# Kernel optimization log

Measured on AMD Instinct MI355X. Metric: run time of the kernel, lower is better.

The kernel has to match this reference:

```python
import jax, jax.numpy as jnp
import numpy as np

NUM_HEADS = 16
NEG = -1e9


def setup_inputs() -> dict:
    key = jax.random.key(0)
    ks = jax.random.split(key, 9)
    B, S, D = 1, 4096, 1024
    s = 1.0 / np.sqrt(D)
    return {
        "x": jax.random.normal(ks[0], (B, S, D), dtype=jnp.float32),
        "wq": jax.random.normal(ks[1], (D, D), dtype=jnp.float32) * s,
        "bq": jax.random.normal(ks[2], (D,), dtype=jnp.float32) * s,
        "wk": jax.random.normal(ks[3], (D, D), dtype=jnp.float32) * s,
        "bk": jax.random.normal(ks[4], (D,), dtype=jnp.float32) * s,
        "wv": jax.random.normal(ks[5], (D, D), dtype=jnp.float32) * s,
        "bv": jax.random.normal(ks[6], (D,), dtype=jnp.float32) * s,
        "wo": jax.random.normal(ks[7], (D, D), dtype=jnp.float32) * s,
        "bo": jax.random.normal(ks[8], (D,), dtype=jnp.float32) * s,
    }


def reference(x, wq, bq, wk, bk, wv, bv, wo, bo):
    B, S, D = x.shape
    H = NUM_HEADS
    hs = D // H
    # torch Linear: y = x @ W^T + b
    q = x @ wq.T + bq
    k = x @ wk.T + bk
    v = x @ wv.T + bv
    # [B, S, D] -> [B, H, S, hs]
    q = q.reshape(B, S, H, hs).transpose(0, 2, 1, 3)
    k = k.reshape(B, S, H, hs).transpose(0, 2, 1, 3)
    v = v.reshape(B, S, H, hs).transpose(0, 2, 1, 3)
    scores = jnp.einsum("bhqd,bhkd->bhqk", q, k) / jnp.sqrt(jnp.asarray(hs, x.dtype))
    causal = jnp.tril(jnp.ones((S, S), dtype=bool))  # True = keep
    scores = jnp.where(causal, scores, jnp.asarray(NEG, x.dtype))
    weights = jax.nn.softmax(scores, axis=-1)
    out = jnp.einsum("bhqk,bhkd->bhqd", weights, v)
    out = out.transpose(0, 2, 1, 3).reshape(B, S, D)
    return out @ wo.T + bo
```

## Files before the change

kernel.cpp:

```cpp
#include <hip/hip_runtime.h>

#define SEQ 4096
#define DM  1024
#define NH  16
#define HS  64
#define LDQK 2048

typedef __attribute__((ext_vector_type(8))) _Float16 f16x8;
typedef __attribute__((ext_vector_type(4))) _Float16 f16x4;
typedef __attribute__((ext_vector_type(4))) float    f32x4;

#define MFMA16(a, b, c) __builtin_amdgcn_mfma_f32_16x16x32_f16((a), (b), (c), 0, 0, 0)

#define DPP_ROR_F(x, N) __int_as_float(__builtin_amdgcn_update_dpp( \
    0, __float_as_int(x), 0x120 + (N), 0xF, 0xF, false))

__device__ __forceinline__ float red16_add(float x) {
    x += DPP_ROR_F(x, 1);
    x += DPP_ROR_F(x, 2);
    x += DPP_ROR_F(x, 4);
    x += DPP_ROR_F(x, 8);
    return x;
}

__global__ __launch_bounds__(256) void cast_all(
    const float* __restrict__ x,
    const float* __restrict__ wq, const float* __restrict__ wk,
    const float* __restrict__ wv, const float* __restrict__ wo,
    _Float16* __restrict__ xb, _Float16* __restrict__ wqkb,
    _Float16* __restrict__ wvb, _Float16* __restrict__ wob)
{
    const float* s; _Float16* d; int i;
    if (blockIdx.y == 0) {
        s = x; d = xb;
        i = blockIdx.x * 1024 + threadIdx.x * 4;
    } else {
        int wsel = blockIdx.x >> 10;
        int bx   = blockIdx.x & 1023;
        switch (wsel) {
            case 0:  s = wq; d = wqkb;               break;
            case 1:  s = wk; d = wqkb + (1u << 20);  break;
            case 2:  s = wv; d = wvb;                break;
            default: s = wo; d = wob;                break;
        }
        i = bx * 1024 + threadIdx.x * 4;
    }
    float4 v = *reinterpret_cast<const float4*>(s + i);
    f16x4 o = {(_Float16)v.x, (_Float16)v.y, (_Float16)v.z, (_Float16)v.w};
    *reinterpret_cast<f16x4*>(d + i) = o;
}

#define GPAD 72

template <int BIAS_ROW, typename OUT_T>
__global__ __launch_bounds__(256, 2) void gemm_bt_f16(
    const _Float16* __restrict__ A,
    const _Float16* __restrict__ W,
    const float*    __restrict__ bias_lo,
    const float*    __restrict__ bias_hi,
    OUT_T* __restrict__ C,
    int M, int N, int K,
    float scale_lo, float scale_hi, int nsplit)
{
    __shared__ _Float16 As[64][GPAD];
    __shared__ _Float16 Bs[128][GPAD];

    const int t    = threadIdx.x;
    const int w    = t >> 6;
    const int lane = t & 63;
    const int q    = lane >> 4;
    const int l    = lane & 15;
    const int m0   = blockIdx.y * 64;
    const int n0   = blockIdx.x * 128;
    const int wm   = (w & 1) * 32;
    const int wn   = (w >> 1) * 64;

    const float* bias  = (n0 < nsplit) ? bias_lo : bias_hi;
    const int    nbase = (n0 < nsplit) ? 0 : nsplit;
    const float  scale = (n0 < nsplit) ? scale_lo : scale_hi;

    const int ar = t >> 2, ac = (t & 3) * 16;
    const int br = t >> 1, bc = (t & 1) * 32;
    const _Float16* gA = A + (size_t)(m0 + ar) * K + ac;
    const _Float16* gW = W + (size_t)(n0 + br) * K + bc;

    uint4 ra0 = *reinterpret_cast<const uint4*>(gA);
    uint4 ra1 = *reinterpret_cast<const uint4*>(gA + 8);
    uint4 rb0 = *reinterpret_cast<const uint4*>(gW);
    uint4 rb1 = *reinterpret_cast<const uint4*>(gW + 8);
    uint4 rb2 = *reinterpret_cast<const uint4*>(gW + 16);
    uint4 rb3 = *reinterpret_cast<const uint4*>(gW + 24);

    f32x4 acc[2][4];
    #pragma unroll
    for (int i = 0; i < 2; ++i)
        #pragma unroll
        for (int j = 0; j < 4; ++j) acc[i][j] = (f32x4){0.f, 0.f, 0.f, 0.f};

    for (int k0 = 0; k0 < K; k0 += 64) {
        __syncthreads();
        *reinterpret_cast<uint4*>(&As[ar][ac])      = ra0;
        *reinterpret_cast<uint4*>(&As[ar][ac + 8])  = ra1;
        *reinterpret_cast<uint4*>(&Bs[br][bc])      = rb0;
        *reinterpret_cast<uint4*>(&Bs[br][bc + 8])  = rb1;
        *reinterpret_cast<uint4*>(&Bs[br][bc + 16]) = rb2;
        *reinterpret_cast<uint4*>(&Bs[br][bc + 24]) = rb3;
        if (k0 + 64 < K) {
            ra0 = *reinterpret_cast<const uint4*>(gA + k0 + 64);
            ra1 = *reinterpret_cast<const uint4*>(gA + k0 + 72);
            rb0 = *reinterpret_cast<const uint4*>(gW + k0 + 64);
            rb1 = *reinterpret_cast<const uint4*>(gW + k0 + 72);
            rb2 = *reinterpret_cast<const uint4*>(gW + k0 + 80);
            rb3 = *reinterpret_cast<const uint4*>(gW + k0 + 88);
        }
        __syncthreads();

        #pragma unroll
        for (int ks = 0; ks < 64; ks += 32) {
            f16x8 af[2], bf[4];
            #pragma unroll
            for (int i = 0; i < 2; ++i)
                af[i] = *reinterpret_cast<const f16x8*>(&As[wm + i * 16 + l][ks + q * 8]);
            #pragma unroll
            for (int j = 0; j < 4; ++j)
                bf[j] = *reinterpret_cast<const f16x8*>(&Bs[wn + j * 16 + l][ks + q * 8]);
            #pragma unroll
            for (int i = 0; i < 2; ++i)
                #pragma unroll
                for (int j = 0; j < 4; ++j)
                    acc[i][j] = MFMA16(af[i], bf[j], acc[i][j]);
        }
    }

    #pragma unroll
    for (int i = 0; i < 2; ++i) {
        #pragma unroll
        for (int j = 0; j < 4; ++j) {
            int gnb = n0 + wn + j * 16 + l;
            float bc2 = BIAS_ROW ? 0.f : bias[gnb - nbase];
            #pragma unroll
            for (int r = 0; r < 4; ++r) {
                int gm = m0 + wm + i * 16 + q * 4 + r;
                float bb = BIAS_ROW ? bias[gm] : bc2;
                C[(size_t)gm * N + gnb] = (OUT_T)((acc[i][j][r] + bb) * scale);
            }
        }
    }
}

#define APAD 72

__global__ __launch_bounds__(256, 2) void attn_mfma(
    const _Float16* __restrict__ Qg,
    const _Float16* __restrict__ Kg,
    const _Float16* __restrict__ Vt,
    _Float16* __restrict__ O)
{
    __shared__ _Float16 QP[128][APAD];
    __shared__ _Float16 Ks[4][16][APAD];
    __shared__ _Float16 Vs[64][APAD];

    const int t    = threadIdx.x;
    const int h    = blockIdx.x;
    const int by   = blockIdx.y;
    const int qb   = (by < 16) ? by : 47 - by;
    const int w    = t >> 6;
    const int lane = t & 63;
    const int q    = lane >> 4;
    const int l    = lane & 15;
    const int sr   = t >> 3;
    const int sc   = (t & 7) * 8;
    const int kj   = sr & 3;
    const int kn   = sr >> 2;

    #pragma unroll
    for (int rr = 0; rr < 4; ++rr)
        *reinterpret_cast<uint4*>(&QP[sr + rr * 32][sc]) =
            *reinterpret_cast<const uint4*>(
                Qg + (size_t)(qb * 128 + sr + rr * 32) * LDQK + h * 64 + sc);

    uint4 kr0 = *reinterpret_cast<const uint4*>(Kg + (size_t)(sr) * LDQK + h * 64 + sc);
    uint4 kr1 = *reinterpret_cast<const uint4*>(Kg + (size_t)(sr + 32) * LDQK + h * 64 + sc);
    uint4 vr0 = *reinterpret_cast<const uint4*>(Vt + (size_t)(h * 64 + sr) * SEQ + sc);
    uint4 vr1 = *reinterpret_cast<const uint4*>(Vt + (size_t)(h * 64 + sr + 32) * SEQ + sc);

    float l_acc[2][4];
    f32x4 oacc[2][4];
    #pragma unroll
    for (int i = 0; i < 2; ++i)
        #pragma unroll
        for (int nt = 0; nt < 4; ++nt) {
            oacc[i][nt] = (f32x4){0.f, 0.f, 0.f, 0.f};
            l_acc[i][nt] = 0.f;
        }

    __syncthreads();
    f16x8 aq[2][2];
    #pragma unroll
    for (int i = 0; i < 2; ++i) {
        aq[i][0] = *reinterpret_cast<const f16x8*>(&QP[w * 32 + i * 16 + l][q * 8]);
        aq[i][1] = *reinterpret_cast<const f16x8*>(&QP[w * 32 + i * 16 + l][32 + q * 8]);
    }

    const int ktmax = 2 * qb + 1;

    for (int kt = 0; kt <= ktmax; ++kt) {
        __syncthreads();
        *reinterpret_cast<uint4*>(&Ks[kj][kn][sc])     = kr0;
        *reinterpret_cast<uint4*>(&Ks[kj][kn + 8][sc]) = kr1;
        *reinterpret_cast<uint4*>(&Vs[sr][sc])         = vr0;
        *reinterpret_cast<uint4*>(&Vs[sr + 32][sc])    = vr1;
        if (kt < ktmax) {
            kr0 = *reinterpret_cast<const uint4*>(
                Kg + (size_t)((kt + 1) * 64 + sr) * LDQK + h * 64 + sc);
            kr1 = *reinterpret_cast<const uint4*>(
                Kg + (size_t)((kt + 1) * 64 + sr + 32) * LDQK + h * 64 + sc);
            vr0 = *reinterpret_cast<const uint4*>(
                Vt + (size_t)(h * 64 + sr) * SEQ + (kt + 1) * 64 + sc);
            vr1 = *reinterpret_cast<const uint4*>(
                Vt + (size_t)(h * 64 + sr + 32) * SEQ + (kt + 1) * 64 + sc);
        }
        __syncthreads();

        f32x4 s0[4], s1[4];
        __builtin_amdgcn_s_setprio(1);
        #pragma unroll
        for (int jt = 0; jt < 4; ++jt) {
            f16x8 bk0 = *reinterpret_cast<const f16x8*>(&Ks[jt][l][q * 8]);
            f16x8 bk1 = *reinterpret_cast<const f16x8*>(&Ks[jt][l][32 + q * 8]);
            f32x4 z0 = (f32x4){0.f, 0.f, 0.f, 0.f};
            z0 = MFMA16(aq[0][0], bk0, z0);
            z0 = MFMA16(aq[0][1], bk1, z0);
            s0[jt] = z0;
            f32x4 z1 = (f32x4){0.f, 0.f, 0.f, 0.f};
            z1 = MFMA16(aq[1][0], bk0, z1);
            z1 = MFMA16(aq[1][1], bk1, z1);
            s1[jt] = z1;
        }
        __builtin_amdgcn_s_setprio(0);

        const bool need_mask = (kt >= 2 * qb);

        #pragma unroll
        for (int i = 0; i < 2; ++i) {
            #pragma unroll
            for (int r = 0; r < 4; ++r) {
                float p0 = (i ? s1 : s0)[0][r], p1 = (i ? s1 : s0)[1][r];
                float p2 = (i ? s1 : s0)[2][r], p3 = (i ? s1 : s0)[3][r];
                if (need_mask) {
                    const int qg = qb * 128 + w * 32 + i * 16 + q * 4 + r;
                    const int kg = kt * 64 + 4 * l;
                    p0 = (kg + 0 <= qg) ? p0 : -1e30f;
                    p1 = (kg + 1 <= qg) ? p1 : -1e30f;
                    p2 = (kg + 2 <= qg) ? p2 : -1e30f;
                    p3 = (kg + 3 <= qg) ? p3 : -1e30f;
                }
                p0 = __builtin_amdgcn_exp2f(p0 - 4.f);
                p1 = __builtin_amdgcn_exp2f(p1 - 4.f);
                p2 = __builtin_amdgcn_exp2f(p2 - 4.f);
                p3 = __builtin_amdgcn_exp2f(p3 - 4.f);
                l_acc[i][r] += (p0 + p1) + (p2 + p3);
                f16x4 pk = {(_Float16)p0, (_Float16)p1, (_Float16)p2, (_Float16)p3};
                *reinterpret_cast<f16x4*>(&QP[w * 32 + i * 16 + q * 4 + r][4 * l]) = pk;
            }
        }

        f16x8 ap[2][2];
        #pragma unroll
        for (int i = 0; i < 2; ++i) {
            ap[i][0] = *reinterpret_cast<const f16x8*>(&QP[w * 32 + i * 16 + l][q * 8]);
            ap[i][1] = *reinterpret_cast<const f16x8*>(&QP[w * 32 + i * 16 + l][32 + q * 8]);
        }
        __builtin_amdgcn_s_setprio(1);
        #pragma unroll
        for (int nt = 0; nt < 4; ++nt) {
            f16x8 bv0 = *reinterpret_cast<const f16x8*>(&Vs[nt * 16 + l][q * 8]);
            f16x8 bv1 = *reinterpret_cast<const f16x8*>(&Vs[nt * 16 + l][32 + q * 8]);
            oacc[0][nt] = MFMA16(ap[0][0], bv0, oacc[0][nt]);
            oacc[0][nt] = MFMA16(ap[0][1], bv1, oacc[0][nt]);
            oacc[1][nt] = MFMA16(ap[1][0], bv0, oacc[1][nt]);
            oacc[1][nt] = MFMA16(ap[1][1], bv1, oacc[1][nt]);
        }
        __builtin_amdgcn_s_setprio(0);
    }

    #pragma unroll
    for (int i = 0; i < 2; ++i) {
        #pragma unroll
        for (int r = 0; r < 4; ++r) {
            float inv = 1.f / red16_add(l_acc[i][r]);
            size_t row = (size_t)(qb * 128 + w * 32 + i * 16 + q * 4 + r) * DM + h * 64;
            #pragma unroll
            for (int nt = 0; nt < 4; ++nt)
                O[row + nt * 16 + l] = (_Float16)(oacc[i][nt][r] * inv);
        }
    }
}

extern "C" void kernel_launch(void* const* d_in, const int* in_sizes, int n_in,
                              void* d_out, int out_size, void* d_ws, size_t ws_size,
                              hipStream_t stream)
{
    const float* x  = (const float*)d_in[0];
    const float* wq = (const float*)d_in[1];
    const float* bq = (const float*)d_in[2];
    const float* wk = (const float*)d_in[3];
    const float* bk = (const float*)d_in[4];
    const float* wv = (const float*)d_in[5];
    const float* bv = (const float*)d_in[6];
    const float* wo = (const float*)d_in[7];
    const float* bo = (const float*)d_in[8];
    float* out = (float*)d_out;

    char* ws = (char*)d_ws;
    _Float16* xb   = (_Float16*)(ws);
    _Float16* wqkb = (_Float16*)(ws + (8ull  << 20));
    _Float16* wvb  = (_Float16*)(ws + (12ull << 20));
    _Float16* wob  = (_Float16*)(ws + (14ull << 20));
    _Float16* QKb  = (_Float16*)(ws + (16ull << 20));
    _Float16* Vtb  = (_Float16*)(ws + (32ull << 20));
    _Float16* Ab   = (_Float16*)(ws + (40ull << 20));

    cast_all<<<dim3(SEQ * DM / 1024, 2), dim3(256), 0, stream>>>(
        x, wq, wk, wv, wo, xb, wqkb, wvb, wob);

    gemm_bt_f16<0, _Float16><<<dim3(2048 / 128, SEQ / 64), dim3(256), 0, stream>>>(
        xb, wqkb, bq, bk, QKb, SEQ, 2048, DM,
        0.18033688011112042f, 1.0f, 1024);

    gemm_bt_f16<1, _Float16><<<dim3(SEQ / 128, DM / 64), dim3(256), 0, stream>>>(
        wvb, xb, bv, bv, Vtb, DM, SEQ, DM, 1.0f, 1.0f, 1 << 30);

    attn_mfma<<<dim3(NH, 32), dim3(256), 0, stream>>>(QKb, QKb + 1024, Vtb, Ab);

    gemm_bt_f16<0, float><<<dim3(DM / 128, SEQ / 64), dim3(256), 0, stream>>>(
        Ab, wob, bo, bo, out, SEQ, DM, DM, 1.0f, 1.0f, 1 << 30);
}
```

Baseline: 226.6 us.

## Split attention KV range across two 256-thread halves per block and merge partials

```diff
diff --git a/kernel.cpp b/kernel.cpp
--- a/kernel.cpp
+++ b/kernel.cpp
@@ -150,39 +150,50 @@
 
 #define APAD 72
 
-__global__ __launch_bounds__(256, 2) void attn_mfma(
+__global__ __launch_bounds__(512, 4) void attn_mfma(
     const _Float16* __restrict__ Qg,
     const _Float16* __restrict__ Kg,
     const _Float16* __restrict__ Vt,
     _Float16* __restrict__ O)
 {
-    __shared__ _Float16 QP[128][APAD];
-    __shared__ _Float16 Ks[4][16][APAD];
-    __shared__ _Float16 Vs[64][APAD];
+    __shared__ __align__(16) char smem[73728];
+    _Float16 (*QPa)[APAD]     = reinterpret_cast<_Float16(*)[APAD]>(smem);
+    _Float16 (*Pb)[APAD]      = reinterpret_cast<_Float16(*)[APAD]>(smem + 18432);
+    _Float16 (*KsB)[16][APAD] = reinterpret_cast<_Float16(*)[16][APAD]>(smem + 36864);
+    _Float16 (*VsB)[APAD]     = reinterpret_cast<_Float16(*)[APAD]>(smem + 46080);
+    _Float16 (*KsA)[16][APAD] = reinterpret_cast<_Float16(*)[16][APAD]>(smem + 55296);
+    _Float16 (*VsA)[APAD]     = reinterpret_cast<_Float16(*)[APAD]>(smem + 64512);
 
     const int t    = threadIdx.x;
     const int h    = blockIdx.x;
     const int by   = blockIdx.y;
-    const int qb   = (by < 16) ? by : 47 - by;
-    const int w    = t >> 6;
+    const int qt   = (by < 16) ? by : 47 - by;
+    const int hb   = t >> 8;
+    const int sub  = (t >> 6) & 3;
     const int lane = t & 63;
     const int q    = lane >> 4;
     const int l    = lane & 15;
-    const int sr   = t >> 3;
-    const int sc   = (t & 7) * 8;
+    const int tt   = t & 255;
+    const int sr   = tt >> 3;
+    const int sc   = (tt & 7) * 8;
     const int kj   = sr & 3;
     const int kn   = sr >> 2;
 
-    #pragma unroll
-    for (int rr = 0; rr < 4; ++rr)
-        *reinterpret_cast<uint4*>(&QP[sr + rr * 32][sc]) =
-            *reinterpret_cast<const uint4*>(
-                Qg + (size_t)(qb * 128 + sr + rr * 32) * LDQK + h * 64 + sc);
-
-    uint4 kr0 = *reinterpret_cast<const uint4*>(Kg + (size_t)(sr) * LDQK + h * 64 + sc);
-    uint4 kr1 = *reinterpret_cast<const uint4*>(Kg + (size_t)(sr + 32) * LDQK + h * 64 + sc);
-    uint4 vr0 = *reinterpret_cast<const uint4*>(Vt + (size_t)(h * 64 + sr) * SEQ + sc);
-    uint4 vr1 = *reinterpret_cast<const uint4*>(Vt + (size_t)(h * 64 + sr + 32) * SEQ + sc);
+    _Float16 (*Ks)[16][APAD] = hb ? KsB : KsA;
+    _Float16 (*Vs)[APAD]     = hb ? VsB : VsA;
+    _Float16 (*Pp)[APAD]     = hb ? Pb  : QPa;
+
+    const int qsr = t >> 2, qsc = (t & 3) * 16;
+    *reinterpret_cast<uint4*>(&QPa[qsr][qsc]) =
+        *reinterpret_cast<const uint4*>(Qg + (size_t)(qt * 128 + qsr) * LDQK + h * 64 + qsc);
+    *reinterpret_cast<uint4*>(&QPa[qsr][qsc + 8]) =
+        *reinterpret_cast<const uint4*>(Qg + (size_t)(qt * 128 + qsr) * LDQK + h * 64 + qsc + 8);
+
+    const int kt0 = hb ? (qt + 1) : 0;
+    uint4 kr0 = *reinterpret_cast<const uint4*>(Kg + (size_t)(kt0 * 64 + sr) * LDQK + h * 64 + sc);
+    uint4 kr1 = *reinterpret_cast<const uint4*>(Kg + (size_t)(kt0 * 64 + sr + 32) * LDQK + h * 64 + sc);
+    uint4 vr0 = *reinterpret_cast<const uint4*>(Vt + (size_t)(h * 64 + sr) * SEQ + kt0 * 64 + sc);
+    uint4 vr1 = *reinterpret_cast<const uint4*>(Vt + (size_t)(h * 64 + sr + 32) * SEQ + kt0 * 64 + sc);
 
     float l_acc[2][4];
     f32x4 oacc[2][4];
@@ -194,23 +205,29 @@
             l_acc[i][nt] = 0.f;
         }
 
-    __syncthreads();
+    asm volatile("s_waitcnt lgkmcnt(0)" ::: "memory");
+    __builtin_amdgcn_s_barrier();
+    __builtin_amdgcn_sched_barrier(0);
+
     f16x8 aq[2][2];
     #pragma unroll
     for (int i = 0; i < 2; ++i) {
-        aq[i][0] = *reinterpret_cast<const f16x8*>(&QP[w * 32 + i * 16 + l][q * 8]);
-        aq[i][1] = *reinterpret_cast<const f16x8*>(&QP[w * 32 + i * 16 + l][32 + q * 8]);
-    }
-
-    const int ktmax = 2 * qb + 1;
-
-    for (int kt = 0; kt <= ktmax; ++kt) {
-        __syncthreads();
+        aq[i][0] = *reinterpret_cast<const f16x8*>(&QPa[sub * 32 + i * 16 + l][q * 8]);
+        aq[i][1] = *reinterpret_cast<const f16x8*>(&QPa[sub * 32 + i * 16 + l][32 + q * 8]);
+    }
+
+    for (int it = 0; it <= qt; ++it) {
+        const int kt = kt0 + it;
+
+        __builtin_amdgcn_sched_barrier(0);
+        __builtin_amdgcn_s_barrier();
+        __builtin_amdgcn_sched_barrier(0);
+
         *reinterpret_cast<uint4*>(&Ks[kj][kn][sc])     = kr0;
         *reinterpret_cast<uint4*>(&Ks[kj][kn + 8][sc]) = kr1;
         *reinterpret_cast<uint4*>(&Vs[sr][sc])         = vr0;
         *reinterpret_cast<uint4*>(&Vs[sr + 32][sc])    = vr1;
-        if (kt < ktmax) {
+        if (it < qt) {
             kr0 = *reinterpret_cast<const uint4*>(
                 Kg + (size_t)((kt + 1) * 64 + sr) * LDQK + h * 64 + sc);
             kr1 = *reinterpret_cast<const uint4*>(
@@ -220,7 +237,9 @@
             vr1 = *reinterpret_cast<const uint4*>(
                 Vt + (size_t)(h * 64 + sr + 32) * SEQ + (kt + 1) * 64 + sc);
         }
-        __syncthreads();
+        asm volatile("s_waitcnt lgkmcnt(0)" ::: "memory");
+        __builtin_amdgcn_s_barrier();
+        __builtin_amdgcn_sched_barrier(0);
 
         f32x4 s0[4], s1[4];
         __builtin_amdgcn_s_setprio(1);
@@ -239,7 +258,7 @@
         }
         __builtin_amdgcn_s_setprio(0);
 
-        const bool need_mask = (kt >= 2 * qb);
+        const bool need_mask = (kt >= 2 * qt);
 
         #pragma unroll
         for (int i = 0; i < 2; ++i) {
@@ -248,7 +267,7 @@
                 float p0 = (i ? s1 : s0)[0][r], p1 = (i ? s1 : s0)[1][r];
                 float p2 = (i ? s1 : s0)[2][r], p3 = (i ? s1 : s0)[3][r];
                 if (need_mask) {
-                    const int qg = qb * 128 + w * 32 + i * 16 + q * 4 + r;
+                    const int qg = qt * 128 + sub * 32 + i * 16 + q * 4 + r;
                     const int kg = kt * 64 + 4 * l;
                     p0 = (kg + 0 <= qg) ? p0 : -1e30f;
                     p1 = (kg + 1 <= qg) ? p1 : -1e30f;
@@ -261,15 +280,15 @@
                 p3 = __builtin_amdgcn_exp2f(p3 - 4.f);
                 l_acc[i][r] += (p0 + p1) + (p2 + p3);
                 f16x4 pk = {(_Float16)p0, (_Float16)p1, (_Float16)p2, (_Float16)p3};
-                *reinterpret_cast<f16x4*>(&QP[w * 32 + i * 16 + q * 4 + r][4 * l]) = pk;
+                *reinterpret_cast<f16x4*>(&Pp[sub * 32 + i * 16 + q * 4 + r][4 * l]) = pk;
             }
         }
 
         f16x8 ap[2][2];
         #pragma unroll
         for (int i = 0; i < 2; ++i) {
-            ap[i][0] = *reinterpret_cast<const f16x8*>(&QP[w * 32 + i * 16 + l][q * 8]);
-            ap[i][1] = *reinterpret_cast<const f16x8*>(&QP[w * 32 + i * 16 + l][32 + q * 8]);
+            ap[i][0] = *reinterpret_cast<const f16x8*>(&Pp[sub * 32 + i * 16 + l][q * 8]);
+            ap[i][1] = *reinterpret_cast<const f16x8*>(&Pp[sub * 32 + i * 16 + l][32 + q * 8]);
         }
         __builtin_amdgcn_s_setprio(1);
         #pragma unroll
@@ -284,15 +303,39 @@
         __builtin_amdgcn_s_setprio(0);
     }
 
-    #pragma unroll
-    for (int i = 0; i < 2; ++i) {
-        #pragma unroll
-        for (int r = 0; r < 4; ++r) {
-            float inv = 1.f / red16_add(l_acc[i][r]);
-            size_t row = (size_t)(qb * 128 + w * 32 + i * 16 + q * 4 + r) * DM + h * 64;
-            #pragma unroll
-            for (int nt = 0; nt < 4; ++nt)
-                O[row + nt * 16 + l] = (_Float16)(oacc[i][nt][r] * inv);
+    float* Xf = reinterpret_cast<float*>(smem + 18432);
+    float* Xl = reinterpret_cast<float*>(smem + 52224);
+
+    __syncthreads();
+    if (hb) {
+        #pragma unroll
+        for (int i = 0; i < 2; ++i) {
+            #pragma unroll
+            for (int r = 0; r < 4; ++r) {
+                float lb = red16_add(l_acc[i][r]);
+                int row = sub * 32 + i * 16 + q * 4 + r;
+                if (l == 0) Xl[row] = lb;
+                #pragma unroll
+                for (int nt = 0; nt < 4; ++nt)
+                    Xf[row * 66 + nt * 16 + l] = oacc[i][nt][r];
+            }
+        }
+    }
+    __syncthreads();
+    if (!hb) {
+        #pragma unroll
+        for (int i = 0; i < 2; ++i) {
+            #pragma unroll
+            for (int r = 0; r < 4; ++r) {
+                int row = sub * 32 + i * 16 + q * 4 + r;
+                float lsum = red16_add(l_acc[i][r]) + Xl[row];
+                float inv = 1.f / lsum;
+                size_t grow = (size_t)(qt * 128 + row) * DM + h * 64;
+                #pragma unroll
+                for (int nt = 0; nt < 4; ++nt)
+                    O[grow + nt * 16 + l] =
+                        (_Float16)((oacc[i][nt][r] + Xf[row * 66 + nt * 16 + l]) * inv);
+            }
         }
     }
 }
@@ -331,7 +374,7 @@
     gemm_bt_f16<1, _Float16><<<dim3(SEQ / 128, DM / 64), dim3(256), 0, stream>>>(
         wvb, xb, bv, bv, Vtb, DM, SEQ, DM, 1.0f, 1.0f, 1 << 30);
 
-    attn_mfma<<<dim3(NH, 32), dim3(256), 0, stream>>>(QKb, QKb + 1024, Vtb, Ab);
+    attn_mfma<<<dim3(NH, 32), dim3(512), 0, stream>>>(QKb, QKb + 1024, Vtb, Ab);
 
     gemm_bt_f16<0, float><<<dim3(DM / 128, SEQ / 64), dim3(256), 0, stream>>>(
         Ab, wob, bo, bo, out, SEQ, DM, DM, 1.0f, 1.0f, 1 << 30);
```

After: 236.6 us. 4.4% more time.
